# Performance work log

Hardware: AMD Instinct MI355X
Metric: run time of the kernel (lower is better)

The kernel has to match this reference:

```python
import jax, jax.numpy as jnp
import numpy as np
import math

B, N, M, Lx = 8, 32, 16, 32
D, TE_DIM, IN_DIM, TT = 64, 16, 17, 63   # hid_dim, te_dim, 1+te_dim, hid_dim-1
H, DH, NL = 4, 16, 2
TAU, DELTA = 60.0, 300.0                 # tau, 5 minutes in seconds
P = B * N * M


def _ln(x, g, b):
    mu = x.mean(-1, keepdims=True)
    v = ((x - mu) ** 2).mean(-1, keepdims=True)
    return (x - mu) / jnp.sqrt(v + 1e-5) * g + b


def _time_bias():
    idx = jnp.arange(M)
    dist = jnp.abs(idx[:, None] - idx[None, :]).astype(jnp.float32) * DELTA
    return jnp.log(jnp.exp(-dist / TAU) + 1e-12)


def _pos_enc():
    pos = jnp.arange(M, dtype=jnp.float32)[:, None]
    div = jnp.exp(jnp.arange(0, D, 2, dtype=jnp.float32) * (-math.log(10000.0) / D))
    pe = jnp.zeros((M, D))
    pe = pe.at[:, 0::2].set(jnp.sin(pos * div))
    pe = pe.at[:, 1::2].set(jnp.cos(pos * div))
    return pe


def _heads(t):   # (b, m, D) -> (b, H, m, DH)
    b, m, _ = t.shape
    return t.reshape(b, m, H, DH).transpose(0, 2, 1, 3)


def _merge(t):   # (b, H, m, DH) -> (b, m, D)
    b, _, m, _ = t.shape
    return t.transpose(0, 2, 1, 3).reshape(b, m, D)


def _patch_gattn(x, pm, qw, qb, kw, kb, vw, vb, ow, ob, tbias):
    q, k, v = _heads(x @ qw.T + qb), _heads(x @ kw.T + kb), _heads(x @ vw.T + vb)
    a = jnp.einsum('bhqd,bhkd->bhqk', q, k) / math.sqrt(DH) + tbias[None, None]
    a = jnp.where((pm == 0.0)[:, None, None, :], -1e9, a)
    out = _merge(jnp.einsum('bhqk,bhkd->bhqd', jax.nn.softmax(a, -1), v))
    return (out @ ow.T + ob) * pm[..., None]


def _mha(q_in, kv_in, in_w, in_b, ow, ob, kpm=None):
    wq, wk, wv = in_w[:D], in_w[D:2 * D], in_w[2 * D:]
    bq, bk, bv = in_b[:D], in_b[D:2 * D], in_b[2 * D:]
    q = _heads(q_in @ wq.T + bq)
    k = _heads(kv_in @ wk.T + bk)
    v = _heads(kv_in @ wv.T + bv)
    a = jnp.einsum('bhqd,bhkd->bhqk', q, k) / math.sqrt(DH)
    if kpm is not None:
        a = jnp.where(kpm[:, None, None, :], -1e9, a)
    out = _merge(jnp.einsum('bhqk,bhkd->bhqd', jax.nn.softmax(a, -1), v))
    return out @ ow.T + ob


def _forward(x, mask, ttcn_w1, ttcn_b1, ttcn_w2, ttcn_b2, ttcn_w3, ttcn_b3, t_bias,
             ga_qw, ga_qb, ga_kw, ga_kb, ga_vw, ga_vb, ga_ow, ga_ob,
             tf_in_w, tf_in_b, tf_out_w, tf_out_b, tf_ln1_g, tf_ln1_b, tf_ln2_g, tf_ln2_b,
             tf_fw1, tf_fb1, tf_fw2, tf_fb2,
             q_embed, cls_in_w, cls_in_b, cls_out_w, cls_out_b, logit_w, logit_b):
    m = mask.astype(x.dtype)                          # (P, Lx, 1)
    # --- TTCN: per-sample dynamic filter generation + masked seq-softmax agg ---
    h = jax.nn.relu(x @ ttcn_w1.T + ttcn_b1)
    h = jax.nn.relu(h @ ttcn_w2.T + ttcn_b2)
    filt = h @ ttcn_w3.T + ttcn_b3                    # (P, Lx, IN_DIM*TT)
    filt = filt * m + (1.0 - m) * (-1e8)
    fs = jax.nn.softmax(filt, axis=1).reshape(P, Lx, TT, IN_DIM)
    h_t = jax.nn.relu(jnp.einsum('pli,plti->pt', x, fs) + t_bias)   # (P, TT)
    mask_patch = (m.sum(axis=1) > 0).astype(x.dtype)  # (P, 1)
    xp = jnp.concatenate([h_t, mask_patch], -1).reshape(B, N, M, D)
    pm = mask_patch.reshape(B, N, M)
    tbias = _time_bias()
    pe = _pos_enc()
    xc = xp
    for l in range(NL):
        if l > 0:
            x_last = xc
        xb = xc.reshape(B * N, M, D)
        pmb = pm.reshape(B * N, M)
        xb = xb + _patch_gattn(xb, pmb, ga_qw[l], ga_qb[l], ga_kw[l], ga_kb[l],
                               ga_vw[l], ga_vb[l], ga_ow[l], ga_ob[l], tbias)
        xb = xb + pe[None]
        # post-norm TransformerEncoderLayer (tf_layer = 1, no attn mask, eval mode)
        attn = _mha(xb, xb, tf_in_w[l], tf_in_b[l], tf_out_w[l], tf_out_b[l])
        xb = _ln(xb + attn, tf_ln1_g[l], tf_ln1_b[l])
        ff = jax.nn.relu(xb @ tf_fw1[l].T + tf_fb1[l]) @ tf_fw2[l].T + tf_fb2[l]
        xb = _ln(xb + ff, tf_ln2_g[l], tf_ln2_b[l])
        xc = xb.reshape(B, N, M, D)
        if l > 0:
            xc = x_last + xc
    x_seq = xc.mean(axis=1)                            # (B, M, D)
    kpm = ~((pm > 0).any(axis=1))                      # (B, M), True = padded
    qs = jnp.broadcast_to(q_embed[None], (B, 5, D))
    z = _mha(qs, x_seq, cls_in_w, cls_in_b, cls_out_w, cls_out_b, kpm=kpm)
    return (z @ logit_w.T + logit_b)[..., 0]           # (B, 5)


def setup_inputs() -> dict:
    key = jax.random.key(0)
    ks = iter(jax.random.split(key, 64))
    def rn(shape, s=0.1):
        return jax.random.normal(next(ks), shape, jnp.float32) * s
    inp = {
        'x': jax.random.normal(next(ks), (P, Lx, IN_DIM), jnp.float32),
        'mask': jax.random.randint(next(ks), (P, Lx, 1), 0, 2, jnp.int32),
        'ttcn_w1': rn((TT, IN_DIM)), 'ttcn_b1': jnp.zeros((TT,)),
        'ttcn_w2': rn((TT, TT)), 'ttcn_b2': jnp.zeros((TT,)),
        'ttcn_w3': rn((IN_DIM * TT, TT)), 'ttcn_b3': jnp.zeros((IN_DIM * TT,)),
        't_bias': rn((1, TT)),
        'ga_qw': rn((NL, D, D)), 'ga_qb': jnp.zeros((NL, D)),
        'ga_kw': rn((NL, D, D)), 'ga_kb': jnp.zeros((NL, D)),
        'ga_vw': rn((NL, D, D)), 'ga_vb': jnp.zeros((NL, D)),
        'ga_ow': rn((NL, D, D)), 'ga_ob': jnp.zeros((NL, D)),
        'tf_in_w': rn((NL, 3 * D, D)), 'tf_in_b': jnp.zeros((NL, 3 * D)),
        'tf_out_w': rn((NL, D, D)), 'tf_out_b': jnp.zeros((NL, D)),
        'tf_ln1_g': jnp.ones((NL, D)), 'tf_ln1_b': jnp.zeros((NL, D)),
        'tf_ln2_g': jnp.ones((NL, D)), 'tf_ln2_b': jnp.zeros((NL, D)),
        'tf_fw1': rn((NL, 2048, D)), 'tf_fb1': jnp.zeros((NL, 2048)),
        'tf_fw2': rn((NL, D, 2048)), 'tf_fb2': jnp.zeros((NL, D)),
        'q_embed': rn((5, D), 1.0),
        'cls_in_w': rn((3 * D, D)), 'cls_in_b': jnp.zeros((3 * D,)),
        'cls_out_w': rn((D, D)), 'cls_out_b': jnp.zeros((D,)),
        'logit_w': rn((1, D)), 'logit_b': jnp.zeros((1,)),
    }
    return inp


def reference(x, mask, ttcn_w1, ttcn_b1, ttcn_w2, ttcn_b2, ttcn_w3, ttcn_b3, t_bias,
              ga_qw, ga_qb, ga_kw, ga_kb, ga_vw, ga_vb, ga_ow, ga_ob,
              tf_in_w, tf_in_b, tf_out_w, tf_out_b, tf_ln1_g, tf_ln1_b, tf_ln2_g, tf_ln2_b,
              tf_fw1, tf_fb1, tf_fw2, tf_fb2,
              q_embed, cls_in_w, cls_in_b, cls_out_w, cls_out_b, logit_w, logit_b):
    return _forward(x, mask, ttcn_w1, ttcn_b1, ttcn_w2, ttcn_b2, ttcn_w3, ttcn_b3, t_bias,
                    ga_qw, ga_qb, ga_kw, ga_kb, ga_vw, ga_vb, ga_ow, ga_ob,
                    tf_in_w, tf_in_b, tf_out_w, tf_out_b, tf_ln1_g, tf_ln1_b, tf_ln2_g, tf_ln2_b,
                    tf_fw1, tf_fb1, tf_fw2, tf_fb2,
                    q_embed, cls_in_w, cls_in_b, cls_out_w, cls_out_b, logit_w, logit_b)
```

## Files before the change

kernel.cpp:

```cpp
#include <hip/hip_runtime.h>
#include <hip/hip_bf16.h>
#include <math.h>

#define B_  8
#define N_  32
#define M_  16
#define LX  32
#define D_  64
#define IN_DIM_ 17
#define TT_ 63
#define H_  4
#define DH_ 16
#define P_TOT 4096
#define BN_ 256
#define FF_ 2048

#define FRAG_TOT 83200
#define OFF_INW  2048
#define OFF_OUTW 3584
#define OFF_FW1  4096
#define OFF_FW2  20480

typedef unsigned short ushort_t;
typedef __attribute__((ext_vector_type(8))) short short8;
typedef __attribute__((ext_vector_type(4))) float floatx4;

#define MFMA16(a,b,c) __builtin_amdgcn_mfma_f32_16x16x32_bf16((a),(b),(c),0,0,0)

__device__ __forceinline__ float fast_exp2(float x){
#if __has_builtin(__builtin_amdgcn_exp2f)
  return __builtin_amdgcn_exp2f(x);
#else
  return __expf(x * 0.6931471805599453f);
#endif
}
__device__ __forceinline__ float fast_rcp(float x){
#if __has_builtin(__builtin_amdgcn_rcpf)
  return __builtin_amdgcn_rcpf(x);
#else
  return 1.0f / x;
#endif
}

__device__ __forceinline__ ushort_t f2bf(float f){
  unsigned u = __float_as_uint(f);
  u += 0x7FFFu + ((u >> 16) & 1u);
  return (ushort_t)(u >> 16);
}
__device__ __forceinline__ float bf2f(ushort_t h){ return __uint_as_float(((unsigned)h) << 16); }

__device__ __forceinline__ uint4 pack8(const ushort_t* h){
  uint4 u;
  u.x = (unsigned)h[0] | ((unsigned)h[1] << 16);
  u.y = (unsigned)h[2] | ((unsigned)h[3] << 16);
  u.z = (unsigned)h[4] | ((unsigned)h[5] << 16);
  u.w = (unsigned)h[6] | ((unsigned)h[7] << 16);
  return u;
}

__device__ __forceinline__ void split8(const float* r, short8& hi, short8& lo){
  #pragma unroll
  for (int j = 0; j < 8; ++j){
    float v = r[j];
    ushort_t h = f2bf(v);
    ushort_t l2 = f2bf(v - bf2f(h));
    hi[j] = (short)h; lo[j] = (short)l2;
  }
}
__device__ __forceinline__ uint4 cvt8(const float* r){
  ushort_t hh[8];
  #pragma unroll
  for (int j = 0; j < 8; ++j) hh[j] = f2bf(r[j]);
  return pack8(hh);
}
__device__ __forceinline__ short8 cvt8s(const float* r){
  union { uint4 u4; short8 s8; } cv;
  cv.u4 = cvt8(r);
  return cv.s8;
}

__device__ __forceinline__ floatx4 mm3(short8 ah, short8 al, short8 bh, short8 bl, floatx4 c){
  c = MFMA16(ah, bh, c); c = MFMA16(ah, bl, c); c = MFMA16(al, bh, c); return c;
}

__device__ __forceinline__ float dot64(const float* __restrict__ a, const float* __restrict__ w){
  const float4* a4 = (const float4*)a;
  const float4* w4 = (const float4*)w;
  float acc = 0.f;
  #pragma unroll
  for (int k = 0; k < 16; ++k){ float4 x = a4[k], y = w4[k];
    acc += x.x*y.x + x.y*y.y + x.z*y.z + x.w*y.w; }
  return acc;
}
__device__ __forceinline__ float dot16(const float* __restrict__ a, const float* __restrict__ b){
  const float4* a4 = (const float4*)a; const float4* b4 = (const float4*)b;
  float acc = 0.f;
  #pragma unroll
  for (int k = 0; k < 4; ++k){ float4 x = a4[k], y = b4[k];
    acc += x.x*y.x + x.y*y.y + x.z*y.z + x.w*y.w; }
  return acc;
}

__device__ __forceinline__ void packA68(const float* buf, short8* fA, int tid){
  if (tid < 128){
    int ln = tid & 63, ks = tid >> 6;
    const float* r = buf + (ln & 15)*68 + ks*32 + ((ln >> 4) & 3)*8;
    short8 hi, lo; split8(r, hi, lo);
    fA[tid] = hi; fA[128 + tid] = lo;
  }
}

__global__ __launch_bounds__(256) void prep_kernel(
    const float* __restrict__ w1, const float* __restrict__ w2, const float* __restrict__ w3,
    const float* __restrict__ gqw, const float* __restrict__ gkw,
    const float* __restrict__ gvw, const float* __restrict__ gow,
    const float* __restrict__ inw, const float* __restrict__ outw,
    const float* __restrict__ fw1, const float* __restrict__ fw2,
    uint4* __restrict__ fr)
{
  int s = blockIdx.x*256 + threadIdx.x;
  if (s >= FRAG_TOT) return;
  const float* src; int Nr, Kr, KS, rel; int w3seg = 0, noLo = 0;
  if (s < 256)      { src = w1; Nr=63;  Kr=17; KS=1; rel = s; noLo = 1; }
  else if (s < 768) { src = w2; Nr=63;  Kr=63; KS=2; rel = s-256; noLo = 1; }
  else if (s < 9472){ src = w3; Nr=1071;Kr=63; KS=2; rel = s-768; w3seg = 1; noLo = 1; }
  else {
    int t = s - 9472, l = t / 36864, r2 = t - l*36864;
    if (r2 < 512)        { src = gqw + l*4096;   Nr=64;  Kr=64;   KS=2;  rel = r2; }
    else if (r2 < 1024)  { src = gkw + l*4096;   Nr=64;  Kr=64;   KS=2;  rel = r2-512; }
    else if (r2 < 1536)  { src = gvw + l*4096;   Nr=64;  Kr=64;   KS=2;  rel = r2-1024; }
    else if (r2 < 2048)  { src = gow + l*4096;   Nr=64;  Kr=64;   KS=2;  rel = r2-1536; }
    else if (r2 < 3584)  { src = inw + l*12288;  Nr=192; Kr=64;   KS=2;  rel = r2-2048; }
    else if (r2 < 4096)  { src = outw + l*4096;  Nr=64;  Kr=64;   KS=2;  rel = r2-3584; }
    else if (r2 < 20480) { src = fw1 + l*131072; Nr=2048;Kr=64;   KS=2;  rel = r2-4096; noLo = 1; }
    else                 { src = fw2 + l*131072; Nr=64;  Kr=2048; KS=64; rel = r2-20480; noLo = 1; }
  }
  int lane = rel & 63, tmp = rel >> 6;
  int ks = tmp % KS, nt = tmp / KS;
  int kb = ks*32 + ((lane >> 4) & 3)*8;
  int n, validn;
  if (w3seg){
    int i = nt >> 2, tq = nt & 3;
    int t = tq*16 + (lane & 15);
    n = t*17 + i;
    validn = (t < 63);
  } else {
    n = nt*16 + (lane & 15);
    validn = (n < Nr);
  }
  float v[8];
  #pragma unroll
  for (int j = 0; j < 8; ++j){
    v[j] = (validn && (kb + j) < Kr) ? src[n*Kr + kb + j] : 0.f;
    if (w3seg){
      if ((kb + j) == 63) v[j] = 1.0f;
      v[j] *= 1.4426950408889634f;
    }
  }
  ushort_t hh[8];
  #pragma unroll
  for (int j = 0; j < 8; ++j) hh[j] = f2bf(v[j]);
  fr[s] = pack8(hh);
  if (!noLo){
    ushort_t ll[8];
    #pragma unroll
    for (int j = 0; j < 8; ++j) ll[j] = f2bf(v[j] - bf2f(hh[j]));
    fr[FRAG_TOT + s] = pack8(ll);
  }
}

__global__ __launch_bounds__(256) void ttcn_kernel(
    const float* __restrict__ x, const int* __restrict__ mask,
    const float* __restrict__ b1, const float* __restrict__ b2,
    const float* __restrict__ tb,
    const short8* __restrict__ w1bhi,
    const short8* __restrict__ w2bhi,
    const short8* __restrict__ w3bhi,
    float* __restrict__ xp, float* __restrict__ pm)
{
  __shared__ __align__(16) char pool[26880];
  float*  xs    = (float*)(pool + 0);
  float*  msv   = (float*)(pool + 2560);
  float*  xsumv = (float*)(pool + 2688);
  short8* xfhi  = (short8*)(pool + 2768);
  float*  h1t   = (float*)(pool + 4816);
  short8* h2fhi = (short8*)(pool + 4816);
  float*  colres= (float*)(pool + 8912);
  float*  h2t   = (float*)(pool + 13776);
  short8* h1fhi = (short8*)(pool + 22736);

  const int p = blockIdx.x, tid = threadIdx.x;
  const int lane = tid & 63, wvi = tid >> 6;
  const int nidx = lane & 15, quad = lane >> 4;

  for (int idx = tid; idx < LX*IN_DIM_; idx += 256){
    int l = (idx * 3856) >> 16;
    int i = idx - l*17;
    xs[l*20 + i] = x[p*(LX*IN_DIM_) + idx];
  }
  if (tid < LX) msv[tid] = (float)mask[p*LX + tid];
  __syncthreads();

  if (tid < 128){
    int mt = tid >> 6;
    int l = mt*16 + nidx;
    float r[8];
    #pragma unroll
    for (int j = 0; j < 8; ++j){
      int k = quad*8 + j;
      r[j] = (k < IN_DIM_) ? xs[l*20 + k] : 0.f;
    }
    ((uint4*)xfhi)[tid] = cvt8(r);
  } else if (tid < 128 + IN_DIM_){
    int i = tid - 128;
    float s = 0.f;
    #pragma unroll
    for (int l = 0; l < LX; ++l) s += xs[l*20 + i];
    xsumv[i] = s;
  }
  __syncthreads();

  {
    short8 axh0 = xfhi[lane], axh1 = xfhi[64 + lane];
    short8 bh = w1bhi[wvi*64 + lane];
    floatx4 a0 = {0.f,0.f,0.f,0.f}, a1 = {0.f,0.f,0.f,0.f};
    a0 = MFMA16(axh0, bh, a0);
    a1 = MFMA16(axh1, bh, a1);
    int t = wvi*16 + nidx;
    float bb = (t < TT_) ? b1[t] : 0.f;
    #pragma unroll
    for (int r = 0; r < 4; ++r){
      h1t[t*35 + quad*4 + r]      = fmaxf(a0[r] + bb, 0.f);
      h1t[t*35 + 16 + quad*4 + r] = fmaxf(a1[r] + bb, 0.f);
    }
  }
  __syncthreads();

  {
    int mt = tid >> 7, ks = (tid >> 6) & 1;
    int l = mt*16 + nidx;
    float r[8];
    #pragma unroll
    for (int j = 0; j < 8; ++j) r[j] = h1t[(ks*32 + quad*8 + j)*35 + l];
    ((uint4*)h1fhi)[tid] = cvt8(r);
  }
  __syncthreads();

  {
    short8 ah00 = h1fhi[lane],       ah01 = h1fhi[64 + lane];
    short8 ah10 = h1fhi[128 + lane], ah11 = h1fhi[192 + lane];
    short8 bh0 = w2bhi[(wvi*2+0)*64 + lane];
    short8 bh1 = w2bhi[(wvi*2+1)*64 + lane];
    floatx4 a0 = {0.f,0.f,0.f,0.f}, a1 = {0.f,0.f,0.f,0.f};
    a0 = MFMA16(ah00, bh0, a0); a0 = MFMA16(ah01, bh1, a0);
    a1 = MFMA16(ah10, bh0, a1); a1 = MFMA16(ah11, bh1, a1);
    int t = wvi*16 + nidx;
    float bb = (t < TT_) ? b2[t] : 0.f;
    #pragma unroll
    for (int r = 0; r < 4; ++r){
      h2t[t*35 + quad*4 + r]      = fmaxf(a0[r] + bb, 0.f);
      h2t[t*35 + 16 + quad*4 + r] = fmaxf(a1[r] + bb, 0.f);
    }
  }
  __syncthreads();

  {
    int mt = tid >> 7, ks = (tid >> 6) & 1;
    int l = mt*16 + nidx;
    float r[8];
    #pragma unroll
    for (int j = 0; j < 8; ++j) r[j] = h2t[(ks*32 + quad*8 + j)*35 + l];
    if (ks == 1 && quad == 3) r[7] = (msv[l] == 0.f) ? -1e8f : 0.f;
    ((uint4*)h2fhi)[tid] = cvt8(r);
  }
  __syncthreads();

  {
    short8 ah00 = h2fhi[lane],       ah01 = h2fhi[64 + lane];
    short8 ah10 = h2fhi[128 + lane], ah11 = h2fhi[192 + lane];
    const int t_out = wvi*16 + nidx;
    const bool valid = t_out < 63;
    const int rA = quad*4, rB = quad*4 + 16;
    short8 nbh0 = w3bhi[(wvi*2+0)*64 + lane];
    short8 nbh1 = w3bhi[(wvi*2+1)*64 + lane];
    for (int it = 0; it < 17; ++it){
      short8 bh0 = nbh0, bh1 = nbh1;
      if (it < 16){
        int nt = wvi + it*4 + 4;
        nbh0 = w3bhi[(nt*2+0)*64 + lane];
        nbh1 = w3bhi[(nt*2+1)*64 + lane];
      }
      floatx4 a0 = {0.f,0.f,0.f,0.f}, a1 = {0.f,0.f,0.f,0.f};
      a0 = MFMA16(ah00, bh0, a0); a0 = MFMA16(ah01, bh1, a0);
      a1 = MFMA16(ah10, bh0, a1); a1 = MFMA16(ah11, bh1, a1);

      float den0 = 0.f, den1 = 0.f, num0 = 0.f, num1 = 0.f;
      #pragma unroll
      for (int r = 0; r < 4; ++r){
        float e0 = fast_exp2(a0[r]);
        den0 += e0; num0 = fmaf(e0, xs[(rA + r)*20 + it], num0);
        float e1 = fast_exp2(a1[r]);
        den1 += e1; num1 = fmaf(e1, xs[(rB + r)*20 + it], num1);
      }
      float den = den0 + den1, num = num0 + num1;
      den += __shfl_xor(den, 16, 64); den += __shfl_xor(den, 32, 64);
      num += __shfl_xor(num, 16, 64); num += __shfl_xor(num, 32, 64);
      if (quad == 0 && valid){
        float res = (den > 0.f) ? num * fast_rcp(den) : xsumv[it] * (1.f/32.f);
        colres[it*64 + t_out] = res;
      }
    }
  }
  __syncthreads();

  if (tid < TT_){
    float acc = 0.f;
    #pragma unroll
    for (int i2 = 0; i2 < IN_DIM_; ++i2) acc += colres[i2*64 + tid];
    xp[p*D_ + tid] = fmaxf(acc + tb[tid], 0.f);
  }
  if (tid == TT_){
    float s = 0.f;
    #pragma unroll
    for (int l = 0; l < LX; ++l) s += msv[l];
    float mp = (s > 0.f) ? 1.f : 0.f;
    xp[p*D_ + TT_] = mp;
    pm[p] = mp;
  }
}

__global__ __launch_bounds__(256) void layer12_kernel(
    const float* __restrict__ xin, const float* __restrict__ pm,
    const short8* __restrict__ frS,
    const float* __restrict__ gqb, const float* __restrict__ gkb,
    const float* __restrict__ gvb, const float* __restrict__ gob,
    const float* __restrict__ inb, const float* __restrict__ outb,
    const float* __restrict__ ln1g, const float* __restrict__ ln1b,
    const float* __restrict__ fb1, const float* __restrict__ fb2,
    const float* __restrict__ ln2g, const float* __restrict__ ln2b,
    float* __restrict__ xout)
{
  __shared__ __align__(16) float xb[16*68];
  __shared__ __align__(16) float xb2[16*68];
  __shared__ __align__(16) float q_[16*68];
  __shared__ __align__(16) float k_[16*68];
  __shared__ __align__(16) float v_[16*68];
  __shared__ __align__(16) float ao[16*68];
  __shared__ __align__(16) float ss[1024];
  __shared__ __align__(16) short8 fragA[256];
  __shared__ __align__(16) float hbuf[4*16*36];
  __shared__ __align__(16) float part[4*16*68];
  __shared__ __align__(16) float pe_t[1024];
  __shared__ float tbt[16];
  __shared__ float pmv[16], mur[16], rvr[16];

  const int bn = blockIdx.x, tid = threadIdx.x;
  const int lane = tid & 63, wvi = tid >> 6;
  const int nidx = lane & 15, quad = lane >> 4;
  const float* xin_p = xin + bn*1024;

  for (int o = tid; o < 1024; o += 256) xb[(o>>6)*68 + (o&63)] = xin_p[o];
  if (tid < 16) pmv[tid] = pm[bn*16 + tid];
  for (int o = tid; o < 1024; o += 256){
    int tok = o >> 6, d = o & 63;
    float div = __expf((float)(d & ~1) * (-0.14391156831212793f));
    float arg = (float)tok * div;
    pe_t[o] = (d & 1) ? cosf(arg) : sinf(arg);
  }
  if (tid >= 32 && tid < 48) tbt[tid-32] = logf(expf(-5.0f*(float)(tid-32)) + 1e-12f);
  __syncthreads();

  for (int l = 0; l < 2; ++l){
    const int lbase = 9472 + l*36864;
    const float* gqbL = gqb + l*64;  const float* gkbL = gkb + l*64;
    const float* gvbL = gvb + l*64;  const float* gobL = gob + l*64;
    const float* inbL = inb + l*192; const float* outbL = outb + l*64;
    const float* ln1gL = ln1g + l*64; const float* ln1bL = ln1b + l*64;
    const float* fb1L = fb1 + l*2048; const float* fb2L = fb2 + l*64;
    const float* ln2gL = ln2g + l*64; const float* ln2bL = ln2b + l*64;

    float xres[4];
    #pragma unroll
    for (int kk2 = 0; kk2 < 4; ++kk2){
      int o = tid + kk2*256;
      xres[kk2] = xb[(o>>6)*68 + (o&63)];
    }

    short8 gb[3][4], ob4[4], mb[3][4];
    #pragma unroll
    for (int mat = 0; mat < 3; ++mat){
      int base = lbase + mat*512;
      gb[mat][0] = frS[base + (wvi*2+0)*64 + lane];
      gb[mat][1] = frS[FRAG_TOT + base + (wvi*2+0)*64 + lane];
      gb[mat][2] = frS[base + (wvi*2+1)*64 + lane];
      gb[mat][3] = frS[FRAG_TOT + base + (wvi*2+1)*64 + lane];
    }
    {
      int base = lbase + 1536;
      ob4[0] = frS[base + (wvi*2+0)*64 + lane];
      ob4[1] = frS[FRAG_TOT + base + (wvi*2+0)*64 + lane];
      ob4[2] = frS[base + (wvi*2+1)*64 + lane];
      ob4[3] = frS[FRAG_TOT + base + (wvi*2+1)*64 + lane];
    }
    #pragma unroll
    for (int sel = 0; sel < 3; ++sel){
      int base = lbase + OFF_INW + (sel*4 + wvi)*128;
      mb[sel][0] = frS[base + lane];
      mb[sel][1] = frS[FRAG_TOT + base + lane];
      mb[sel][2] = frS[base + 64 + lane];
      mb[sel][3] = frS[FRAG_TOT + base + 64 + lane];
    }

    packA68(xb, fragA, tid);
    __syncthreads();
    {
      short8 axh0 = fragA[lane], axh1 = fragA[64+lane];
      short8 axl0 = fragA[128+lane], axl1 = fragA[192+lane];
      #pragma unroll
      for (int mat = 0; mat < 3; ++mat){
        floatx4 c = {0.f,0.f,0.f,0.f};
        c = mm3(axh0, axl0, gb[mat][0], gb[mat][1], c);
        c = mm3(axh1, axl1, gb[mat][2], gb[mat][3], c);
        int d = wvi*16 + nidx;
        float bb = (mat == 0 ? gqbL : mat == 1 ? gkbL : gvbL)[d];
        float* dst = (mat == 0 ? q_ : mat == 1 ? k_ : v_);
        #pragma unroll
        for (int r = 0; r < 4; ++r) dst[(quad*4+r)*68 + d] = c[r] + bb;
      }
    }
    __syncthreads();
    {
      int row = tid >> 2;
      int h = row >> 4, qm = row & 15;
      int km0 = (tid & 3) * 4;
      float s4[4];
      #pragma unroll
      for (int j = 0; j < 4; ++j){
        int km = km0 + j;
        float acc = dot16(q_ + qm*68 + h*16, k_ + km*68 + h*16);
        int dd = qm - km; if (dd < 0) dd = -dd;
        acc = acc * 0.25f + tbt[dd];
        if (pmv[km] == 0.f) acc = -1e9f;
        s4[j] = acc;
      }
      float mx = fmaxf(fmaxf(s4[0], s4[1]), fmaxf(s4[2], s4[3]));
      mx = fmaxf(mx, __shfl_xor(mx, 1, 64));
      mx = fmaxf(mx, __shfl_xor(mx, 2, 64));
      float e4[4], se = 0.f;
      #pragma unroll
      for (int j = 0; j < 4; ++j){ e4[j] = __expf(s4[j]-mx); se += e4[j]; }
      se += __shfl_xor(se, 1, 64);
      se += __shfl_xor(se, 2, 64);
      float inv = fast_rcp(se);
      #pragma unroll
      for (int j = 0; j < 4; ++j) ss[row*16 + km0 + j] = e4[j]*inv;
    }
    __syncthreads();
    for (int o = tid; o < 1024; o += 256){
      int m = o >> 6, d = o & 63, h = d >> 4;
      float acc = 0.f;
      #pragma unroll
      for (int km = 0; km < 16; ++km) acc += ss[h*256 + m*16 + km] * v_[km*68 + d];
      ao[m*68 + d] = acc;
    }
    __syncthreads();
    packA68(ao, fragA, tid);
    __syncthreads();
    {
      short8 axh0 = fragA[lane], axh1 = fragA[64+lane];
      short8 axl0 = fragA[128+lane], axl1 = fragA[192+lane];
      floatx4 c = {0.f,0.f,0.f,0.f};
      c = mm3(axh0, axl0, ob4[0], ob4[1], c);
      c = mm3(axh1, axl1, ob4[2], ob4[3], c);
      int d = wvi*16 + nidx;
      float bb = gobL[d];
      #pragma unroll
      for (int r = 0; r < 4; ++r){
        int tok = quad*4 + r;
        xb[tok*68 + d] += (c[r] + bb) * pmv[tok] + pe_t[tok*64 + d];
      }
    }
    __syncthreads();

    short8 mob[4], f1c[4], f2c[4];
    {
      int base = lbase + OFF_OUTW;
      mob[0] = frS[base + (wvi*2+0)*64 + lane];
      mob[1] = frS[FRAG_TOT + base + (wvi*2+0)*64 + lane];
      mob[2] = frS[base + (wvi*2+1)*64 + lane];
      mob[3] = frS[FRAG_TOT + base + (wvi*2+1)*64 + lane];
    }
    {
      int f1base = lbase + OFF_FW1, f2base = lbase + OFF_FW2;
      #pragma unroll
      for (int t2 = 0; t2 < 2; ++t2){
        int sb = f1base + ((wvi*32+t2)*2)*64 + lane;
        f1c[t2*2+0] = frS[sb];
        f1c[t2*2+1] = frS[sb + 64];
      }
      #pragma unroll
      for (int ntd = 0; ntd < 4; ++ntd)
        f2c[ntd] = frS[f2base + (ntd*64 + wvi*16)*64 + lane];
    }

    packA68(xb, fragA, tid);
    __syncthreads();
    {
      short8 axh0 = fragA[lane], axh1 = fragA[64+lane];
      short8 axl0 = fragA[128+lane], axl1 = fragA[192+lane];
      #pragma unroll
      for (int sel = 0; sel < 3; ++sel){
        floatx4 c = {0.f,0.f,0.f,0.f};
        c = mm3(axh0, axl0, mb[sel][0], mb[sel][1], c);
        c = mm3(axh1, axl1, mb[sel][2], mb[sel][3], c);
        int d = wvi*16 + nidx;
        float bb = inbL[(sel*4 + wvi)*16 + nidx];
        float* dst = (sel == 0 ? q_ : sel == 1 ? k_ : v_);
        #pragma unroll
        for (int r = 0; r < 4; ++r) dst[(quad*4+r)*68 + d] = c[r] + bb;
      }
    }
    __syncthreads();
    {
      int row = tid >> 2;
      int h = row >> 4, qm = row & 15;
      int km0 = (tid & 3) * 4;
      float s4[4];
      #pragma unroll
      for (int j = 0; j < 4; ++j)
        s4[j] = 0.25f * dot16(q_ + qm*68 + h*16, k_ + (km0+j)*68 + h*16);
      float mx = fmaxf(fmaxf(s4[0], s4[1]), fmaxf(s4[2], s4[3]));
      mx = fmaxf(mx, __shfl_xor(mx, 1, 64));
      mx = fmaxf(mx, __shfl_xor(mx, 2, 64));
      float e4[4], se = 0.f;
      #pragma unroll
      for (int j = 0; j < 4; ++j){ e4[j] = __expf(s4[j]-mx); se += e4[j]; }
      se += __shfl_xor(se, 1, 64);
      se += __shfl_xor(se, 2, 64);
      float inv = fast_rcp(se);
      #pragma unroll
      for (int j = 0; j < 4; ++j) ss[row*16 + km0 + j] = e4[j]*inv;
    }
    __syncthreads();
    for (int o = tid; o < 1024; o += 256){
      int m = o >> 6, d = o & 63, h = d >> 4;
      float acc = 0.f;
      #pragma unroll
      for (int km = 0; km < 16; ++km) acc += ss[h*256 + m*16 + km] * v_[km*68 + d];
      ao[m*68 + d] = acc;
    }
    __syncthreads();
    packA68(ao, fragA, tid);
    __syncthreads();
    {
      short8 axh0 = fragA[lane], axh1 = fragA[64+lane];
      short8 axl0 = fragA[128+lane], axl1 = fragA[192+lane];
      floatx4 c = {0.f,0.f,0.f,0.f};
      c = mm3(axh0, axl0, mob[0], mob[1], c);
      c = mm3(axh1, axl1, mob[2], mob[3], c);
      int d = wvi*16 + nidx;
      float bb = outbL[d];
      #pragma unroll
      for (int r = 0; r < 4; ++r) xb[(quad*4+r)*68 + d] += c[r] + bb;
    }
    __syncthreads();

    if (tid < 64){
      int row = tid >> 2, seg = tid & 3;
      const float* rp = xb + row*68 + seg*16;
      float s = 0.f;
      #pragma unroll
      for (int j = 0; j < 16; ++j) s += rp[j];
      s += __shfl_xor(s, 1, 64); s += __shfl_xor(s, 2, 64);
      float mu = s * (1.f/64.f);
      float v = 0.f;
      #pragma unroll
      for (int j = 0; j < 16; ++j){ float t = rp[j]-mu; v += t*t; }
      v += __shfl_xor(v, 1, 64); v += __shfl_xor(v, 2, 64);
      if (seg == 0){ mur[row] = mu; rvr[row] = rsqrtf(v*(1.f/64.f) + 1e-5f); }
    }
    __syncthreads();
    for (int o = tid; o < 1024; o += 256){
      int m = o >> 6, d = o & 63;
      xb2[m*68 + d] = (xb[m*68 + d] - mur[m]) * rvr[m] * ln1gL[d] + ln1bL[d];
    }
    __syncthreads();
    packA68(xb2, fragA, tid);
    __syncthreads();

    {
      const int w = wvi;
      const int f1base = lbase + OFF_FW1, f2base = lbase + OFF_FW2;
      short8 axh0 = fragA[lane], axh1 = fragA[64 + lane];
      floatx4 y0 = {0.f,0.f,0.f,0.f}, y1 = y0, y2 = y0, y3 = y0;
      float* hw = hbuf + w*576;

      short8 f1n[4], f2n[4];
      for (int it = 0; it < 16; ++it){
        int ntA = w*32 + it*2;
        floatx4 hA = {0.f,0.f,0.f,0.f}, hB = hA;
        hA = MFMA16(axh0, f1c[0], hA); hA = MFMA16(axh1, f1c[1], hA);
        hB = MFMA16(axh0, f1c[2], hB); hB = MFMA16(axh1, f1c[3], hB);
        float bbA = fb1L[ntA*16 + nidx], bbB = fb1L[ntA*16 + 16 + nidx];
        #pragma unroll
        for (int r = 0; r < 4; ++r){
          hw[(quad*4+r)*36 + nidx]      = fmaxf(hA[r] + bbA, 0.f);
          hw[(quad*4+r)*36 + 16 + nidx] = fmaxf(hB[r] + bbB, 0.f);
        }
        if (it < 15){
          int ntN = ntA + 2, kstN = w*16 + it + 1;
          #pragma unroll
          for (int t2 = 0; t2 < 2; ++t2){
            int sb = f1base + ((ntN+t2)*2)*64 + lane;
            f1n[t2*2+0] = frS[sb];
            f1n[t2*2+1] = frS[sb + 64];
          }
          #pragma unroll
          for (int ntd = 0; ntd < 4; ++ntd)
            f2n[ntd] = frS[f2base + (ntd*64 + kstN)*64 + lane];
        }
        short8 ah = cvt8s(hw + (lane & 15)*36 + quad*8);
        y0 = MFMA16(ah, f2c[0], y0);
        y1 = MFMA16(ah, f2c[1], y1);
        y2 = MFMA16(ah, f2c[2], y2);
        y3 = MFMA16(ah, f2c[3], y3);
        #pragma unroll
        for (int j = 0; j < 4; ++j){ f1c[j] = f1n[j]; f2c[j] = f2n[j]; }
      }
      #pragma unroll
      for (int r = 0; r < 4; ++r){
        int row = (quad*4 + r)*68;
        part[w*1088 + row + nidx]      = y0[r];
        part[w*1088 + row + 16 + nidx] = y1[r];
        part[w*1088 + row + 32 + nidx] = y2[r];
        part[w*1088 + row + 48 + nidx] = y3[r];
      }
    }
    __syncthreads();
    for (int o = tid; o < 1024; o += 256){
      int tok = o >> 6, d = o & 63;
      float s = xb2[tok*68 + d] + fb2L[d];
      #pragma unroll
      for (int ww = 0; ww < 4; ++ww) s += part[ww*1088 + tok*68 + d];
      xb[tok*68 + d] = s;
    }
    __syncthreads();
    if (tid < 64){
      int row = tid >> 2, seg = tid & 3;
      const float* rp = xb + row*68 + seg*16;
      float s = 0.f;
      #pragma unroll
      for (int j = 0; j < 16; ++j) s += rp[j];
      s += __shfl_xor(s, 1, 64); s += __shfl_xor(s, 2, 64);
      float mu = s * (1.f/64.f);
      float v = 0.f;
      #pragma unroll
      for (int j = 0; j < 16; ++j){ float t = rp[j]-mu; v += t*t; }
      v += __shfl_xor(v, 1, 64); v += __shfl_xor(v, 2, 64);
      if (seg == 0){ mur[row] = mu; rvr[row] = rsqrtf(v*(1.f/64.f) + 1e-5f); }
    }
    __syncthreads();
    #pragma unroll
    for (int kk2 = 0; kk2 < 4; ++kk2){
      int o = tid + kk2*256;
      int tok = o >> 6, d = o & 63;
      float vv = (xb[tok*68 + d] - mur[tok]) * rvr[tok] * ln2gL[d] + ln2bL[d];
      if (l == 0) xb[tok*68 + d] = vv;
      else        xout[bn*1024 + o] = vv + xres[kk2];
    }
    __syncthreads();
  }
}

__global__ __launch_bounds__(256) void final_kernel(
    const float* __restrict__ xc, const float* __restrict__ pm,
    const float* __restrict__ q_embed,
    const float* __restrict__ cin_w, const float* __restrict__ cin_b,
    const float* __restrict__ cout_w, const float* __restrict__ cout_b,
    const float* __restrict__ logit_w, const float* __restrict__ logit_b,
    float* __restrict__ out)
{
  const int b = blockIdx.x;
  const int tid = threadIdx.x;
  __shared__ __align__(16) float xs[M_ * D_];
  __shared__ float kpmv[M_];
  __shared__ __align__(16) float qv[5 * D_], kv[M_ * D_], vv[M_ * D_];
  __shared__ float sv[H_ * 5 * M_];
  __shared__ __align__(16) float ao[5 * D_], zv[5 * D_];

  for (int o = tid; o < M_ * D_; o += 256) {
    int m = o >> 6, d = o & 63;
    float acc = 0.f;
    #pragma unroll
    for (int n = 0; n < N_; ++n) acc += xc[(((b * N_ + n) * M_ + m) * D_) + d];
    xs[o] = acc * (1.f / 32.f);
  }
  if (tid < M_) {
    float any = 0.f;
    #pragma unroll
    for (int n = 0; n < N_; ++n) any += (pm[(b * N_ + n) * M_ + tid] > 0.f) ? 1.f : 0.f;
    kpmv[tid] = (any > 0.f) ? 0.f : 1.f;
  }
  __syncthreads();

  for (int o = tid; o < 5 * D_; o += 256) {
    int qi = o >> 6, d = o & 63;
    qv[o] = cin_b[d] + dot64(q_embed + qi * D_, cin_w + d * D_);
  }
  for (int o = tid; o < 2 * M_ * D_; o += 256) {
    int sel = o >> 10, r = o & 1023, m = r >> 6, d = r & 63;
    float acc = cin_b[D_ + sel * D_ + d] + dot64(xs + m * D_, cin_w + (D_ + sel * D_ + d) * D_);
    ((sel == 0) ? kv : vv)[r] = acc;
  }
  __syncthreads();

  for (int o = tid; o < H_ * 5 * M_; o += 256) {
    int h = o / 80, r = o % 80, qi = r >> 4, km = r & 15;
    float acc = 0.25f * dot16(qv + qi * D_ + h * DH_, kv + km * D_ + h * DH_);
    if (kpmv[km] != 0.f) acc = -1e9f;
    sv[o] = acc;
  }
  __syncthreads();
  if (tid < H_ * 5) {
    int h = tid / 5, qi = tid % 5;
    float* row = sv + h * 80 + qi * M_;
    float mx = -1e30f;
    #pragma unroll
    for (int km = 0; km < M_; ++km) mx = fmaxf(mx, row[km]);
    float se = 0.f;
    #pragma unroll
    for (int km = 0; km < M_; ++km) { float e = __expf(row[km] - mx); row[km] = e; se += e; }
    float inv = 1.f / se;
    #pragma unroll
    for (int km = 0; km < M_; ++km) row[km] *= inv;
  }
  __syncthreads();
  for (int o = tid; o < 5 * D_; o += 256) {
    int qi = o >> 6, d = o & 63, h = d >> 4;
    float acc = 0.f;
    #pragma unroll
    for (int km = 0; km < M_; ++km) acc += sv[h * 80 + qi * M_ + km] * vv[km * D_ + d];
    ao[o] = acc;
  }
  __syncthreads();
  for (int o = tid; o < 5 * D_; o += 256) {
    int qi = o >> 6, d = o & 63;
    zv[o] = cout_b[d] + dot64(ao + qi * D_, cout_w + d * D_);
  }
  __syncthreads();
  if (tid < 5) {
    float acc = logit_b[0] + dot64(zv + tid * D_, logit_w);
    out[b * 5 + tid] = acc;
  }
}

extern "C" void kernel_launch(void* const* d_in, const int* in_sizes, int n_in,
                              void* d_out, int out_size, void* d_ws, size_t ws_size,
                              hipStream_t stream) {
  const float* x       = (const float*)d_in[0];
  const int*   mask    = (const int*)  d_in[1];
  const float* ttcn_w1 = (const float*)d_in[2];
  const float* ttcn_b1 = (const float*)d_in[3];
  const float* ttcn_w2 = (const float*)d_in[4];
  const float* ttcn_b2 = (const float*)d_in[5];
  const float* ttcn_w3 = (const float*)d_in[6];
  const float* ttcn_b3 = (const float*)d_in[7];
  const float* t_bias  = (const float*)d_in[8];
  const float* ga_qw   = (const float*)d_in[9];
  const float* ga_qb   = (const float*)d_in[10];
  const float* ga_kw   = (const float*)d_in[11];
  const float* ga_kb   = (const float*)d_in[12];
  const float* ga_vw   = (const float*)d_in[13];
  const float* ga_vb   = (const float*)d_in[14];
  const float* ga_ow   = (const float*)d_in[15];
  const float* ga_ob   = (const float*)d_in[16];
  const float* tf_in_w = (const float*)d_in[17];
  const float* tf_in_b = (const float*)d_in[18];
  const float* tf_out_w= (const float*)d_in[19];
  const float* tf_out_b= (const float*)d_in[20];
  const float* tf_ln1g = (const float*)d_in[21];
  const float* tf_ln1b = (const float*)d_in[22];
  const float* tf_ln2g = (const float*)d_in[23];
  const float* tf_ln2b = (const float*)d_in[24];
  const float* tf_fw1  = (const float*)d_in[25];
  const float* tf_fb1  = (const float*)d_in[26];
  const float* tf_fw2  = (const float*)d_in[27];
  const float* tf_fb2  = (const float*)d_in[28];
  const float* q_embed = (const float*)d_in[29];
  const float* cls_in_w  = (const float*)d_in[30];
  const float* cls_in_b  = (const float*)d_in[31];
  const float* cls_out_w = (const float*)d_in[32];
  const float* cls_out_b = (const float*)d_in[33];
  const float* logit_w = (const float*)d_in[34];
  const float* logit_b = (const float*)d_in[35];
  (void)ttcn_b3;

  float* wsf  = (float*)d_ws;
  float* xp   = wsf;
  float* pmb  = wsf + P_TOT * D_;
  float* xbuf = pmb + P_TOT;
  uint4* fr   = (uint4*)(xbuf + P_TOT * D_);
  const short8* frS = (const short8*)fr;

  prep_kernel<<<325, 256, 0, stream>>>(ttcn_w1, ttcn_w2, ttcn_w3,
      ga_qw, ga_kw, ga_vw, ga_ow, tf_in_w, tf_out_w, tf_fw1, tf_fw2, fr);

  ttcn_kernel<<<P_TOT, 256, 0, stream>>>(x, mask, ttcn_b1, ttcn_b2, t_bias,
      frS + 0, frS + 256, frS + 768,
      xp, pmb);

  layer12_kernel<<<BN_, 256, 0, stream>>>(xp, pmb, frS,
      ga_qb, ga_kb, ga_vb, ga_ob, tf_in_b, tf_out_b, tf_ln1g, tf_ln1b,
      tf_fb1, tf_fb2, tf_ln2g, tf_ln2b, xbuf);

  final_kernel<<<B_, 256, 0, stream>>>(xbuf, pmb, q_embed,
                                       cls_in_w, cls_in_b, cls_out_w, cls_out_b,
                                       logit_w, logit_b, (float*)d_out);
}
```

Before: 235.3 us.

## Store TTCN hidden activations as bf16 in MFMA-ready layout, drop repack passes

The TTCN kernel now writes the layer-1 and layer-2 ReLU outputs straight to shared memory as bf16, in a row layout that the next MFMA can read as short8 fragments. This removes the two intermediate repack stages and their barriers. It also adds a transposed copy of x so the softmax-weighted sum reads float4 vectors instead of strided scalars. Shared memory per block shrinks, which may allow more blocks per CU. The mask value is now injected directly into the fragment register, and the 2-byte strided stores may cause LDS bank conflicts.

```diff
diff --git a/kernel.cpp b/kernel.cpp
--- a/kernel.cpp
+++ b/kernel.cpp
@@ -178,16 +178,15 @@
     const short8* __restrict__ w3bhi,
     float* __restrict__ xp, float* __restrict__ pm)
 {
-  __shared__ __align__(16) char pool[26880];
-  float*  xs    = (float*)(pool + 0);
-  float*  msv   = (float*)(pool + 2560);
-  float*  xsumv = (float*)(pool + 2688);
-  short8* xfhi  = (short8*)(pool + 2768);
-  float*  h1t   = (float*)(pool + 4816);
-  short8* h2fhi = (short8*)(pool + 4816);
-  float*  colres= (float*)(pool + 8912);
-  float*  h2t   = (float*)(pool + 13776);
-  short8* h1fhi = (short8*)(pool + 22736);
+  __shared__ __align__(16) char pool[16512];
+  float*    xs    = (float*)(pool + 0);
+  float*    xst   = (float*)(pool + 2560);
+  float*    msv   = (float*)(pool + 5008);
+  float*    xsumv = (float*)(pool + 5136);
+  short8*   xfhi  = (short8*)(pool + 5216);
+  ushort_t* h1t   = (ushort_t*)(pool + 7264);
+  float*    colres= (float*)(pool + 7264);
+  ushort_t* h2t   = (ushort_t*)(pool + 11872);
 
   const int p = blockIdx.x, tid = threadIdx.x;
   const int lane = tid & 63, wvi = tid >> 6;
@@ -211,12 +210,18 @@
       r[j] = (k < IN_DIM_) ? xs[l*20 + k] : 0.f;
     }
     ((uint4*)xfhi)[tid] = cvt8(r);
-  } else if (tid < 128 + IN_DIM_){
-    int i = tid - 128;
-    float s = 0.f;
-    #pragma unroll
-    for (int l = 0; l < LX; ++l) s += xs[l*20 + i];
-    xsumv[i] = s;
+  } else {
+    if (tid < 128 + IN_DIM_){
+      int i = tid - 128;
+      float s = 0.f;
+      #pragma unroll
+      for (int l = 0; l < LX; ++l) s += xs[l*20 + i];
+      xsumv[i] = s;
+    }
+    for (int idx = tid - 128; idx < 544; idx += 128){
+      int i = idx >> 5, l = idx & 31;
+      xst[i*36 + l] = xs[l*20 + i];
+    }
   }
   __syncthreads();
 
@@ -230,57 +235,52 @@
     float bb = (t < TT_) ? b1[t] : 0.f;
     #pragma unroll
     for (int r = 0; r < 4; ++r){
-      h1t[t*35 + quad*4 + r]      = fmaxf(a0[r] + bb, 0.f);
-      h1t[t*35 + 16 + quad*4 + r] = fmaxf(a1[r] + bb, 0.f);
+      h1t[(quad*4+r)*72 + t]      = f2bf(fmaxf(a0[r] + bb, 0.f));
+      h1t[(16+quad*4+r)*72 + t]   = f2bf(fmaxf(a1[r] + bb, 0.f));
     }
   }
   __syncthreads();
 
   {
-    int mt = tid >> 7, ks = (tid >> 6) & 1;
-    int l = mt*16 + nidx;
-    float r[8];
-    #pragma unroll
-    for (int j = 0; j < 8; ++j) r[j] = h1t[(ks*32 + quad*8 + j)*35 + l];
-    ((uint4*)h1fhi)[tid] = cvt8(r);
-  }
-  __syncthreads();
-
-  {
-    short8 ah00 = h1fhi[lane],       ah01 = h1fhi[64 + lane];
-    short8 ah10 = h1fhi[128 + lane], ah11 = h1fhi[192 + lane];
+    short8 ah[2][2];
+    #pragma unroll
+    for (int mt = 0; mt < 2; ++mt)
+      #pragma unroll
+      for (int ks = 0; ks < 2; ++ks){
+        int l = mt*16 + nidx;
+        ah[mt][ks] = *(const short8*)((const char*)h1t + (l*72 + ks*32 + quad*8)*2);
+      }
     short8 bh0 = w2bhi[(wvi*2+0)*64 + lane];
     short8 bh1 = w2bhi[(wvi*2+1)*64 + lane];
     floatx4 a0 = {0.f,0.f,0.f,0.f}, a1 = {0.f,0.f,0.f,0.f};
-    a0 = MFMA16(ah00, bh0, a0); a0 = MFMA16(ah01, bh1, a0);
-    a1 = MFMA16(ah10, bh0, a1); a1 = MFMA16(ah11, bh1, a1);
+    a0 = MFMA16(ah[0][0], bh0, a0); a0 = MFMA16(ah[0][1], bh1, a0);
+    a1 = MFMA16(ah[1][0], bh0, a1); a1 = MFMA16(ah[1][1], bh1, a1);
     int t = wvi*16 + nidx;
     float bb = (t < TT_) ? b2[t] : 0.f;
     #pragma unroll
     for (int r = 0; r < 4; ++r){
-      h2t[t*35 + quad*4 + r]      = fmaxf(a0[r] + bb, 0.f);
-      h2t[t*35 + 16 + quad*4 + r] = fmaxf(a1[r] + bb, 0.f);
+      h2t[(quad*4+r)*72 + t]      = f2bf(fmaxf(a0[r] + bb, 0.f));
+      h2t[(16+quad*4+r)*72 + t]   = f2bf(fmaxf(a1[r] + bb, 0.f));
     }
   }
   __syncthreads();
 
   {
-    int mt = tid >> 7, ks = (tid >> 6) & 1;
-    int l = mt*16 + nidx;
-    float r[8];
-    #pragma unroll
-    for (int j = 0; j < 8; ++j) r[j] = h2t[(ks*32 + quad*8 + j)*35 + l];
-    if (ks == 1 && quad == 3) r[7] = (msv[l] == 0.f) ? -1e8f : 0.f;
-    ((uint4*)h2fhi)[tid] = cvt8(r);
-  }
-  __syncthreads();
-
-  {
-    short8 ah00 = h2fhi[lane],       ah01 = h2fhi[64 + lane];
-    short8 ah10 = h2fhi[128 + lane], ah11 = h2fhi[192 + lane];
+    short8 ah[2][2];
+    #pragma unroll
+    for (int mt = 0; mt < 2; ++mt)
+      #pragma unroll
+      for (int ks = 0; ks < 2; ++ks){
+        int l = mt*16 + nidx;
+        ah[mt][ks] = *(const short8*)((const char*)h2t + (l*72 + ks*32 + quad*8)*2);
+      }
+    if (quad == 3){
+      ah[0][1][7] = (short)((msv[nidx]      == 0.f) ? f2bf(-1e8f) : (ushort_t)0);
+      ah[1][1][7] = (short)((msv[16 + nidx] == 0.f) ? f2bf(-1e8f) : (ushort_t)0);
+    }
     const int t_out = wvi*16 + nidx;
     const bool valid = t_out < 63;
-    const int rA = quad*4, rB = quad*4 + 16;
+    const int rA = quad*4;
     short8 nbh0 = w3bhi[(wvi*2+0)*64 + lane];
     short8 nbh1 = w3bhi[(wvi*2+1)*64 + lane];
     for (int it = 0; it < 17; ++it){
@@ -291,17 +291,21 @@
         nbh1 = w3bhi[(nt*2+1)*64 + lane];
       }
       floatx4 a0 = {0.f,0.f,0.f,0.f}, a1 = {0.f,0.f,0.f,0.f};
-      a0 = MFMA16(ah00, bh0, a0); a0 = MFMA16(ah01, bh1, a0);
-      a1 = MFMA16(ah10, bh0, a1); a1 = MFMA16(ah11, bh1, a1);
-
+      a0 = MFMA16(ah[0][0], bh0, a0); a0 = MFMA16(ah[0][1], bh1, a0);
+      a1 = MFMA16(ah[1][0], bh0, a1); a1 = MFMA16(ah[1][1], bh1, a1);
+
+      const float4 xA = *(const float4*)(xst + it*36 + rA);
+      const float4 xB = *(const float4*)(xst + it*36 + rA + 16);
       float den0 = 0.f, den1 = 0.f, num0 = 0.f, num1 = 0.f;
-      #pragma unroll
-      for (int r = 0; r < 4; ++r){
-        float e0 = fast_exp2(a0[r]);
-        den0 += e0; num0 = fmaf(e0, xs[(rA + r)*20 + it], num0);
-        float e1 = fast_exp2(a1[r]);
-        den1 += e1; num1 = fmaf(e1, xs[(rB + r)*20 + it], num1);
-      }
+      float e;
+      e = fast_exp2(a0[0]); den0 += e; num0 = fmaf(e, xA.x, num0);
+      e = fast_exp2(a0[1]); den0 += e; num0 = fmaf(e, xA.y, num0);
+      e = fast_exp2(a0[2]); den0 += e; num0 = fmaf(e, xA.z, num0);
+      e = fast_exp2(a0[3]); den0 += e; num0 = fmaf(e, xA.w, num0);
+      e = fast_exp2(a1[0]); den1 += e; num1 = fmaf(e, xB.x, num1);
+      e = fast_exp2(a1[1]); den1 += e; num1 = fmaf(e, xB.y, num1);
+      e = fast_exp2(a1[2]); den1 += e; num1 = fmaf(e, xB.z, num1);
+      e = fast_exp2(a1[3]); den1 += e; num1 = fmaf(e, xB.w, num1);
       float den = den0 + den1, num = num0 + num1;
       den += __shfl_xor(den, 16, 64); den += __shfl_xor(den, 32, 64);
       num += __shfl_xor(num, 16, 64); num += __shfl_xor(num, 32, 64);
```

Result: no change. 234.1 us (-0.5%).
